# Performance work log

Measured on AMD Instinct MI355X. Metric: run time of the kernel, lower is better.

The kernel has to match this reference:

```python
import jax, jax.numpy as jnp
import numpy as np

B, OBS, H, M, L1, T, A = 16384, 376, 512, 8, 3, 50, 17  # L1 = num_layers - 1
LOG_SQRT_2PI = 0.5 * np.log(2.0 * np.pi).astype(np.float32)


def setup_inputs() -> dict:
    key = jax.random.key(0)
    ks = jax.random.split(key, 16)
    s = lambda fan: 1.0 / np.sqrt(fan).astype(np.float32)
    return {
        "x": jax.random.normal(ks[0], (B, OBS), jnp.float32),
        "task_idx": jax.random.randint(ks[1], (B,), 0, T, jnp.int64),
        "enc_W1": jax.random.normal(ks[2], (OBS, H), jnp.float32) * s(OBS),
        "enc_b1": jnp.zeros((H,), jnp.float32),
        "enc_W2": jax.random.normal(ks[3], (H, H), jnp.float32) * s(H),
        "enc_b2": jnp.zeros((H,), jnp.float32),
        "task_emb": jax.random.normal(ks[4], (T, H), jnp.float32),
        "a_rW": jax.random.normal(ks[5], (L1, H, M * M), jnp.float32) * s(H),
        "a_rb": jnp.zeros((L1, M * M), jnp.float32),
        "c_rW": jax.random.normal(ks[6], (L1, H, M * M), jnp.float32) * s(H),
        "c_rb": jnp.zeros((L1, M * M), jnp.float32),
        "a_W": jax.random.normal(ks[7], (L1, M, H, H), jnp.float32) * s(H),
        "a_b": jnp.zeros((L1, M, H), jnp.float32),
        "a_Wf": jax.random.normal(ks[8], (M, H, A), jnp.float32) * 0.01,
        "a_bf": jnp.zeros((M, A), jnp.float32),
        "c_W": jax.random.normal(ks[9], (L1, M, H, H), jnp.float32) * s(H),
        "c_b": jnp.zeros((L1, M, H), jnp.float32),
        "c_Wf": jax.random.normal(ks[10], (M, H, 1), jnp.float32) * s(H),
        "c_bf": jnp.zeros((M, 1), jnp.float32),
        "actor_logstd": jnp.zeros((1, A), jnp.float32),
    }


def _routing(context, rW, rb):
    # context: [B,H]; rW: [L1,H,M*M] -> list of [B,M,M] softmax routing probs
    rel = jax.nn.relu(context)
    probs = []
    for l in range(L1):
        logits = (rel @ rW[l] + rb[l]).reshape(-1, M, M)
        probs.append(jax.nn.softmax(logits, axis=2))
    return probs


def _base(f_s, probs, W, b, Wf, bf):
    # f_s: [B,H]; W: [L1,M,H,H]; Wf: [M,H,out]
    g = jnp.broadcast_to(f_s[:, None, :], (f_s.shape[0], M, H))  # [B,M,H]
    for l in range(L1):
        outs = jax.nn.relu(jnp.einsum("bmh,mhk->bmk", g, W[l]) + b[l])  # [B,M,H]
        g = jnp.einsum("bij,bjh->bih", probs[l], outs)  # soft combine
    final = jnp.einsum("bmh,mhk->bmk", g, Wf) + bf  # [B,M,out]
    return final.sum(axis=1)


def reference(x, task_idx, enc_W1, enc_b1, enc_W2, enc_b2, task_emb,
              a_rW, a_rb, c_rW, c_rb, a_W, a_b, a_Wf, a_bf,
              c_W, c_b, c_Wf, c_bf, actor_logstd):
    f_s = jnp.tanh(jnp.tanh(x @ enc_W1 + enc_b1) @ enc_W2 + enc_b2)  # [B,H]
    h_z = task_emb[task_idx]  # [B,H]
    context = f_s * h_z

    value = _base(f_s, _routing(context, c_rW, c_rb), c_W, c_b, c_Wf, c_bf)  # [B,1]
    mean = _base(f_s, _routing(context, a_rW, a_rb), a_W, a_b, a_Wf, a_bf)   # [B,A]

    # deterministic action (sample=False): action = mean
    logstd = jnp.broadcast_to(actor_logstd, mean.shape)
    log_prob = (-logstd - LOG_SQRT_2PI).sum(axis=1)          # N.log_prob(mean).sum(1)
    entropy = (0.5 + LOG_SQRT_2PI + logstd).sum(axis=1)
    # concat (action, log_prob, entropy, value) -> [B, A+3]
    return jnp.concatenate([mean, log_prob[:, None], entropy[:, None], value], axis=1)
```

## Files before the change

### kernel.cpp

```cpp
#include <hip/hip_runtime.h>
#include <hip/hip_bf16.h>

typedef float f32x4 __attribute__((ext_vector_type(4)));
typedef float f32x2 __attribute__((ext_vector_type(2)));
typedef int   i32x4 __attribute__((ext_vector_type(4)));
typedef int   i32x8 __attribute__((ext_vector_type(8)));

#define LOG_SQRT_2PI 0.91893853320467274f

static constexpr int BSZ  = 16384;
static constexpr int OBSN = 376;
static constexpr int HD   = 512;
static constexpr int NACT = 17;

__device__ __forceinline__ unsigned char f2fp8(float v) {
  return (unsigned char)(__builtin_amdgcn_cvt_pk_fp8_f32(v, v, 0, false) & 0xFF);
}

__device__ __forceinline__ void xcd_map(int id, int gx, int gy, int& bx, int& by, int& bz) {
  int p = id & 7, l = id >> 3;
  bx = l % gx;
  int g = (l / gx) * 8 + p;
  by = g % gy;
  bz = g / gy;
}


__global__ void k_cvt_pad8(const float* __restrict__ src, unsigned char* __restrict__ dst) {
  long i = (long)blockIdx.x * 256 + threadIdx.x;
  if (i >= (long)BSZ * HD) return;
  long r = i >> 9;
  int  c = (int)(i & 511);
  dst[i] = f2fp8(c < OBSN ? src[r * OBSN + c] : 0.f);
}

__global__ void k_packT8(const float* __restrict__ src, unsigned char* __restrict__ dst,
                         int K, int N, int Kpad, long sstride, long dstride, float scale) {
  __shared__ float t[32][33];
  src += (long)blockIdx.z * sstride;
  dst += (long)blockIdx.z * dstride;
  int k0 = blockIdx.y * 32, n0 = blockIdx.x * 32;
#pragma unroll
  for (int ii = 0; ii < 4; ++ii) {
    int i = ii * 8 + threadIdx.y;
    int k = k0 + i, n = n0 + threadIdx.x;
    t[i][threadIdx.x] = (k < K && n < N) ? src[(long)k * N + n] : 0.f;
  }
  __syncthreads();
#pragma unroll
  for (int ii = 0; ii < 4; ++ii) {
    int i = ii * 8 + threadIdx.y;
    int n = n0 + i, k = k0 + threadIdx.x;
    if (n < N && k < Kpad) dst[(long)n * Kpad + k] = f2fp8(scale * t[threadIdx.x][i]);
  }
}

__global__ void k_packw8(const float* __restrict__ aW, const float* __restrict__ cW,
                         unsigned char* __restrict__ dst) {
  __shared__ float t[32][33];
  const int z = blockIdx.z;
  const float* src = (z < 24) ? aW + (long)z * 262144 : cW + (long)(z - 24) * 262144;
  unsigned char* d = dst + (long)z * 262144;
  int k0 = blockIdx.y * 32, n0 = blockIdx.x * 32;
#pragma unroll
  for (int ii = 0; ii < 4; ++ii) {
    int i = ii * 8 + threadIdx.y;
    t[i][threadIdx.x] = src[(long)(k0 + i) * 512 + n0 + threadIdx.x];
  }
  __syncthreads();
#pragma unroll
  for (int ii = 0; ii < 4; ++ii) {
    int i = ii * 8 + threadIdx.y;
    d[(long)(n0 + i) * 512 + k0 + threadIdx.x] = f2fp8(16.f * t[threadIdx.x][i]);
  }
}

__global__ void k_packwf8(const float* __restrict__ aWf, const float* __restrict__ cWf,
                          unsigned char* __restrict__ dsta, unsigned char* __restrict__ dstc) {
  int i = blockIdx.x * 256 + threadIdx.x;
  int n = i >> 12, k = i & 4095;
  dsta[i] = (n < NACT) ? f2fp8(64.f * aWf[(long)k * NACT + n]) : (unsigned char)0;
  dstc[i] = (n < 1)    ? f2fp8(64.f * cWf[k])                  : (unsigned char)0;
}

__global__ void k_pack_rb(const float* __restrict__ a_rb, const float* __restrict__ c_rb,
                          float* __restrict__ rb) {
  int i = threadIdx.x;
  rb[i] = (i < 192) ? a_rb[i] : c_rb[i - 192];
}

__global__ void k_sum_bf(const float* __restrict__ a_bf, const float* __restrict__ c_bf,
                         float* __restrict__ sa, float* __restrict__ sc) {
  int a = threadIdx.x;
  if (a < NACT) { float s = 0.f; for (int m = 0; m < 8; ++m) s += a_bf[m * NACT + a]; sa[a] = s; }
  if (a == 0)   { float s = 0.f; for (int m = 0; m < 8; ++m) s += c_bf[m];            sc[0] = s; }
}

template <int OP>
__global__ __launch_bounds__(256)
void k_gemm8(const unsigned char* __restrict__ A, const unsigned char* __restrict__ Bt,
             void* __restrict__ Cv, const float* __restrict__ bias,
             int N, int K, int lda, int ldc, int gx, int gy,
             int a_zoff, int b_zoff, int c_zoff, int bias_zoff,
             const int* __restrict__ tidx, const float* __restrict__ temb,
             unsigned char* __restrict__ out2) {
  __shared__ alignas(16) unsigned char sA[128 * 128];
  __shared__ alignas(16) unsigned char sB[128 * 128];
  int bx, by, z;
  xcd_map(blockIdx.x, gx, gy, bx, by, z);
  A  += (long)z * a_zoff;
  Bt += (long)z * b_zoff;
  const int tid  = threadIdx.x;
  const int wave = tid >> 6, lane = tid & 63;
  const int wr = (wave >> 1) * 64, wc = (wave & 1) * 64;
  const int row0 = by * 128, col0 = bx * 128;
  const int lcol = lane & 15, quad = lane >> 4;
  const int sw7 = lcol & 7;
  const int c0 = ((2 * quad)     ^ sw7) * 16;
  const int c1 = ((2 * quad + 1) ^ sw7) * 16;

  f32x4 acc[4][4] = {};

  for (int kt = 0; kt < K; kt += 128) {
#pragma unroll
    for (int i = 0; i < 4; ++i) {
      int u = i * 256 + tid;
      int r = u >> 3, gc = (u & 7) ^ (r & 7);
      const unsigned char* ga = A + (long)(row0 + r) * lda + kt + gc * 16;
      __builtin_amdgcn_global_load_lds((const __attribute__((address_space(1))) void*)ga,
                                       (__attribute__((address_space(3))) void*)&sA[u * 16], 16, 0, 0);
    }
#pragma unroll
    for (int i = 0; i < 4; ++i) {
      int u = i * 256 + tid;
      int r = u >> 3, gc = (u & 7) ^ (r & 7);
      const unsigned char* gb = Bt + (long)(col0 + r) * K + kt + gc * 16;
      __builtin_amdgcn_global_load_lds((const __attribute__((address_space(1))) void*)gb,
                                       (__attribute__((address_space(3))) void*)&sB[u * 16], 16, 0, 0);
    }
    __syncthreads();
    i32x8 af[4], bv[4];
#pragma unroll
    for (int t = 0; t < 4; ++t) {
      int ra = (wr + t * 16 + lcol) * 128;
      int rb = (wc + t * 16 + lcol) * 128;
      i32x4 alo = *(const i32x4*)&sA[ra + c0];
      i32x4 ahi = *(const i32x4*)&sA[ra + c1];
      i32x4 blo = *(const i32x4*)&sB[rb + c0];
      i32x4 bhi = *(const i32x4*)&sB[rb + c1];
      af[t] = (i32x8){alo[0], alo[1], alo[2], alo[3], ahi[0], ahi[1], ahi[2], ahi[3]};
      bv[t] = (i32x8){blo[0], blo[1], blo[2], blo[3], bhi[0], bhi[1], bhi[2], bhi[3]};
    }
#pragma unroll
    for (int mi = 0; mi < 4; ++mi)
#pragma unroll
      for (int ni = 0; ni < 4; ++ni)
        acc[mi][ni] = __builtin_amdgcn_mfma_scale_f32_16x16x128_f8f6f4(
            bv[ni], af[mi], acc[mi][ni], 0, 0, 0, 0x7F, 0, 0x7F);
    __syncthreads();
  }

#pragma unroll
  for (int ni = 0; ni < 4; ++ni) {
    int colb = col0 + wc + ni * 16 + quad * 4;
    if (colb >= N) continue;
    float4 bw = *(const float4*)&bias[(long)z * bias_zoff + colb];
#pragma unroll
    for (int mi = 0; mi < 4; ++mi) {
      int rowg = row0 + wr + mi * 16 + lcol;
      float v0 = acc[mi][ni][0] * 0.0625f + bw.x;
      float v1 = acc[mi][ni][1] * 0.0625f + bw.y;
      float v2 = acc[mi][ni][2] * 0.0625f + bw.z;
      float v3 = acc[mi][ni][3] * 0.0625f + bw.w;
      long idx = (long)rowg * ldc + (long)z * c_zoff + colb;
      if (OP == 1) {
        float t0 = tanhf(v0), t1 = tanhf(v1), t2 = tanhf(v2), t3 = tanhf(v3);
        unsigned d = __builtin_amdgcn_cvt_pk_fp8_f32(t0, t1, 0, false);
        d = __builtin_amdgcn_cvt_pk_fp8_f32(t2, t3, d, true);
        *(unsigned*)&((unsigned char*)Cv)[idx] = d;
      } else if (OP == 5) {
        float t0 = tanhf(v0), t1 = tanhf(v1), t2 = tanhf(v2), t3 = tanhf(v3);
        unsigned d = __builtin_amdgcn_cvt_pk_fp8_f32(t0, t1, 0, false);
        d = __builtin_amdgcn_cvt_pk_fp8_f32(t2, t3, d, true);
        *(unsigned*)&((unsigned char*)Cv)[idx] = d;
        int tk = tidx[rowg];
        float4 te = *(const float4*)&temb[(long)tk * HD + colb];
        unsigned e = __builtin_amdgcn_cvt_pk_fp8_f32(fmaxf(t0 * te.x, 0.f), fmaxf(t1 * te.y, 0.f), 0, false);
        e = __builtin_amdgcn_cvt_pk_fp8_f32(fmaxf(t2 * te.z, 0.f), fmaxf(t3 * te.w, 0.f), e, true);
        *(unsigned*)&out2[idx] = e;
      } else if (OP == 4) {
        float mx = fmaxf(fmaxf(v0, v1), fmaxf(v2, v3));
        mx = fmaxf(mx, __shfl_xor(mx, 16));
        float e0 = __expf(v0 - mx), e1 = __expf(v1 - mx), e2 = __expf(v2 - mx), e3 = __expf(v3 - mx);
        float s = e0 + e1 + e2 + e3;
        s += __shfl_xor(s, 16);
        float inv = 1.f / s;
        *(float4*)&((float*)Cv)[idx] = make_float4(e0 * inv, e1 * inv, e2 * inv, e3 * inv);
      }
    }
  }
}

__global__ __launch_bounds__(512, 2)
void k_gemm256(const unsigned char* __restrict__ A, const unsigned char* __restrict__ Bt,
               unsigned char* __restrict__ C, const float* __restrict__ bias,
               int K, int lda, int ldc, int gx, int gy,
               int a_zoff, int b_zoff, int c_zoff, int bias_zoff) {
  __shared__ alignas(16) unsigned char sA[2][256 * 128];
  __shared__ alignas(16) unsigned char sB[2][256 * 128];
  int bx, by, z;
  xcd_map(blockIdx.x, gx, gy, bx, by, z);
  A  += (long)z * a_zoff;
  Bt += (long)z * b_zoff;
  const int tid  = threadIdx.x;
  const int wave = tid >> 6, lane = tid & 63;
  const int wr = (wave >> 2) * 128;
  const int wc = (wave & 3) * 64;
  const int row0 = by * 256, col0 = bx * 256;
  const int lcol = lane & 15, quad = lane >> 4;
  const int sw7 = lcol & 7;
  const int c0 = ((2 * quad)     ^ sw7) * 16;
  const int c1 = ((2 * quad + 1) ^ sw7) * 16;

  f32x4 acc[8][4] = {};

  auto stage = [&](int kt, int p) {
#pragma unroll
    for (int i = 0; i < 4; ++i) {
      int u = i * 512 + tid;
      int r = u >> 3, gc = (u & 7) ^ (r & 7);
      const unsigned char* ga = A + (long)(row0 + r) * lda + kt + gc * 16;
      __builtin_amdgcn_global_load_lds((const __attribute__((address_space(1))) void*)ga,
                                       (__attribute__((address_space(3))) void*)&sA[p][u * 16], 16, 0, 0);
    }
#pragma unroll
    for (int i = 0; i < 4; ++i) {
      int u = i * 512 + tid;
      int r = u >> 3, gc = (u & 7) ^ (r & 7);
      const unsigned char* gb = Bt + (long)(col0 + r) * K + kt + gc * 16;
      __builtin_amdgcn_global_load_lds((const __attribute__((address_space(1))) void*)gb,
                                       (__attribute__((address_space(3))) void*)&sB[p][u * 16], 16, 0, 0);
    }
  };

  stage(0, 0);
  __syncthreads();
  int p = 0;
  for (int kt = 0; kt < K; kt += 128) {
    if (kt + 128 < K) stage(kt + 128, p ^ 1);
    i32x8 bv[4];
#pragma unroll
    for (int ni = 0; ni < 4; ++ni) {
      int rb = (wc + ni * 16 + lcol) * 128;
      i32x4 blo = *(const i32x4*)&sB[p][rb + c0];
      i32x4 bhi = *(const i32x4*)&sB[p][rb + c1];
      bv[ni] = (i32x8){blo[0], blo[1], blo[2], blo[3], bhi[0], bhi[1], bhi[2], bhi[3]};
    }
#pragma unroll
    for (int mi = 0; mi < 8; ++mi) {
      int ra = (wr + mi * 16 + lcol) * 128;
      i32x4 alo = *(const i32x4*)&sA[p][ra + c0];
      i32x4 ahi = *(const i32x4*)&sA[p][ra + c1];
      i32x8 af = (i32x8){alo[0], alo[1], alo[2], alo[3], ahi[0], ahi[1], ahi[2], ahi[3]};
      __builtin_amdgcn_s_setprio(1);
#pragma unroll
      for (int ni = 0; ni < 4; ++ni)
        acc[mi][ni] = __builtin_amdgcn_mfma_scale_f32_16x16x128_f8f6f4(
            bv[ni], af, acc[mi][ni], 0, 0, 0, 0x7F, 0, 0x7F);
      __builtin_amdgcn_s_setprio(0);
    }
    __syncthreads();
    p ^= 1;
  }

#pragma unroll
  for (int ni = 0; ni < 4; ++ni) {
    int colb = col0 + wc + ni * 16 + quad * 4;
    float4 bw = *(const float4*)&bias[(long)z * bias_zoff + colb];
#pragma unroll
    for (int mi = 0; mi < 8; ++mi) {
      int rowg = row0 + wr + mi * 16 + lcol;
      float v0 = fmaxf(acc[mi][ni][0] * 0.0625f + bw.x, 0.f);
      float v1 = fmaxf(acc[mi][ni][1] * 0.0625f + bw.y, 0.f);
      float v2 = fmaxf(acc[mi][ni][2] * 0.0625f + bw.z, 0.f);
      float v3 = fmaxf(acc[mi][ni][3] * 0.0625f + bw.w, 0.f);
      unsigned d = __builtin_amdgcn_cvt_pk_fp8_f32(v0, v1, 0, false);
      d = __builtin_amdgcn_cvt_pk_fp8_f32(v2, v3, d, true);
      *(unsigned*)&C[(long)rowg * ldc + (long)z * c_zoff + colb] = d;
    }
  }
}

__global__ __launch_bounds__(256)
void k_combine8(const unsigned char* __restrict__ outs, const float* __restrict__ probs,
                unsigned char* __restrict__ g, int poff) {
  __shared__ float P[4][64];
  const int w = threadIdx.x >> 6, l = threadIdx.x & 63;
  const long b = (long)blockIdx.x * 4 + w;
  P[w][l] = probs[b * 384 + poff + l];
  __syncthreads();
  const unsigned char* ob = outs + b * 4096 + l * 8;
  float o[8][8];
#pragma unroll
  for (int j = 0; j < 8; ++j) {
    uint2 v = *(const uint2*)(ob + j * 512);
    f32x2 p01 = __builtin_amdgcn_cvt_pk_f32_fp8(v.x, false);
    f32x2 p23 = __builtin_amdgcn_cvt_pk_f32_fp8(v.x, true);
    f32x2 p45 = __builtin_amdgcn_cvt_pk_f32_fp8(v.y, false);
    f32x2 p67 = __builtin_amdgcn_cvt_pk_f32_fp8(v.y, true);
    o[j][0] = p01.x; o[j][1] = p01.y; o[j][2] = p23.x; o[j][3] = p23.y;
    o[j][4] = p45.x; o[j][5] = p45.y; o[j][6] = p67.x; o[j][7] = p67.y;
  }
  unsigned char* gb = g + b * 4096 + l * 8;
#pragma unroll
  for (int i = 0; i < 8; ++i) {
    float a[8] = {};
#pragma unroll
    for (int j = 0; j < 8; ++j) {
      float pw = P[w][i * 8 + j];
#pragma unroll
      for (int c = 0; c < 8; ++c) a[c] += pw * o[j][c];
    }
    unsigned int lo = __builtin_amdgcn_cvt_pk_fp8_f32(a[0], a[1], 0, false);
    lo = __builtin_amdgcn_cvt_pk_fp8_f32(a[2], a[3], lo, true);
    unsigned int hi = __builtin_amdgcn_cvt_pk_fp8_f32(a[4], a[5], 0, false);
    hi = __builtin_amdgcn_cvt_pk_fp8_f32(a[6], a[7], hi, true);
    *(uint2*)(gb + i * 512) = make_uint2(lo, hi);
  }
}

template <int NOUT>
__global__ __launch_bounds__(256)
void k_head8(const unsigned char* __restrict__ A, const unsigned char* __restrict__ Bt,
             const float* __restrict__ bsum, float* __restrict__ out, int ooff) {
  __shared__ alignas(16) unsigned char sA[64 * 64];
  __shared__ alignas(16) unsigned char sB[32 * 64];
  const int tid = threadIdx.x;
  const int wave = tid >> 6, lane = tid & 63;
  const int row0 = blockIdx.x * 64;
  const int lcol = lane & 15, quad = lane >> 4;
  const int sw = (lcol >> 1) & 3;
  const int co0 = (((quad >> 1)    ) ^ sw) * 16 + (quad & 1) * 8;
  const int co1 = (((quad >> 1) + 2) ^ sw) * 16 + (quad & 1) * 8;
  f32x4 acc[2] = {};

  for (int kt = 0; kt < 4096; kt += 64) {
    {
      int r = tid >> 2, gc = (tid & 3) ^ ((tid >> 3) & 3);
      const unsigned char* ga = A + (long)(row0 + r) * 4096 + kt + gc * 16;
      __builtin_amdgcn_global_load_lds((const __attribute__((address_space(1))) void*)ga,
                                       (__attribute__((address_space(3))) void*)&sA[tid * 16], 16, 0, 0);
    }
    if (tid < 128) {
      int r = tid >> 2, gc = (tid & 3) ^ ((tid >> 3) & 3);
      const unsigned char* gb = Bt + (long)r * 4096 + kt + gc * 16;
      __builtin_amdgcn_global_load_lds((const __attribute__((address_space(1))) void*)gb,
                                       (__attribute__((address_space(3))) void*)&sB[tid * 16], 16, 0, 0);
    }
    __syncthreads();
    long af[2], bv[2][2];
    int ra = (wave * 16 + lcol) * 64;
    af[0] = *(const long*)&sA[ra + co0];
    af[1] = *(const long*)&sA[ra + co1];
#pragma unroll
    for (int ni = 0; ni < 2; ++ni) {
      int rb = (ni * 16 + lcol) * 64;
      bv[0][ni] = *(const long*)&sB[rb + co0];
      bv[1][ni] = *(const long*)&sB[rb + co1];
    }
#pragma unroll
    for (int kk = 0; kk < 2; ++kk)
#pragma unroll
      for (int ni = 0; ni < 2; ++ni)
        acc[ni] = __builtin_amdgcn_mfma_f32_16x16x32_fp8_fp8(af[kk], bv[kk][ni], acc[ni], 0, 0, 0);
    __syncthreads();
  }

#pragma unroll
  for (int ni = 0; ni < 2; ++ni) {
    int col = ni * 16 + lcol;
    if (col >= NOUT) continue;
#pragma unroll
    for (int r = 0; r < 4; ++r) {
      int row = row0 + wave * 16 + quad * 4 + r;
      out[(long)row * 20 + ooff + col] = acc[ni][r] * 0.015625f + bsum[col];
    }
  }
}

__global__ void k_logstd(const float* __restrict__ ls, float* __restrict__ out) {
  float lp = 0.f, ent = 0.f;
#pragma unroll
  for (int a = 0; a < NACT; ++a) {
    float v = ls[a];
    lp  += -v - LOG_SQRT_2PI;
    ent += 0.5f + LOG_SQRT_2PI + v;
  }
  long b = (long)blockIdx.x * 256 + threadIdx.x;
  if (b < BSZ) { out[b * 20 + 17] = lp; out[b * 20 + 18] = ent; }
}


extern "C" void kernel_launch(void* const* d_in, const int* in_sizes, int n_in,
                              void* d_out, int out_size, void* d_ws, size_t ws_size,
                              hipStream_t stream) {
  const float* x        = (const float*)d_in[0];
  const int*   task_idx = (const int*)d_in[1];
  const float* enc_W1   = (const float*)d_in[2];
  const float* enc_b1   = (const float*)d_in[3];
  const float* enc_W2   = (const float*)d_in[4];
  const float* enc_b2   = (const float*)d_in[5];
  const float* task_emb = (const float*)d_in[6];
  const float* a_rW     = (const float*)d_in[7];
  const float* a_rb     = (const float*)d_in[8];
  const float* c_rW     = (const float*)d_in[9];
  const float* c_rb     = (const float*)d_in[10];
  const float* a_W      = (const float*)d_in[11];
  const float* a_b      = (const float*)d_in[12];
  const float* a_Wf     = (const float*)d_in[13];
  const float* a_bf     = (const float*)d_in[14];
  const float* c_W      = (const float*)d_in[15];
  const float* c_b      = (const float*)d_in[16];
  const float* c_Wf     = (const float*)d_in[17];
  const float* c_bf     = (const float*)d_in[18];
  const float* logstd   = (const float*)d_in[19];
  float* out = (float*)d_out;

  char* ws = (char*)d_ws;
  size_t off = 0;
  auto carve = [&](size_t bytes) {
    char* p = ws + off;
    off += (bytes + 255) & ~(size_t)255;
    return p;
  };
  unsigned char* W8 = (unsigned char*)carve((size_t)48 * 262144);
  unsigned char* W1T8 = (unsigned char*)carve((size_t)512 * 512);
  unsigned char* W2T8 = (unsigned char*)carve((size_t)512 * 512);
  unsigned char* rWT8 = (unsigned char*)carve((size_t)384 * 512);
  float* rball = (float*)carve(384 * 4);
  unsigned char* WfaT8 = (unsigned char*)carve((size_t)32 * 4096);
  unsigned char* WfcT8 = (unsigned char*)carve((size_t)32 * 4096);
  float* bfa   = (float*)carve(128 * 4);
  float* bfc   = (float*)carve(128 * 4);
  unsigned char* fs8 = (unsigned char*)carve((size_t)BSZ * HD);
  float* lgt   = (float*)carve((size_t)BSZ * 384 * 4);

  size_t remain = (ws_size > off) ? (ws_size - off) : 0;
  int Bc = 4096;
  for (int cand = BSZ; cand > 4096; cand >>= 1)
    if ((size_t)2 * cand * 4096 <= remain) { Bc = cand; break; }
  size_t half = (size_t)Bc * 4096;
  unsigned char* bufA8 = (unsigned char*)carve(half);
  unsigned char* bufB8 = (unsigned char*)carve(half);
  unsigned char* x8   = bufA8;
  unsigned char* h18  = bufB8;
  unsigned char* rel8 = bufA8;

  dim3 tb(32, 8);

  k_cvt_pad8<<<(int)(((long)BSZ * HD + 255) / 256), 256, 0, stream>>>(x, x8);
  k_packT8<<<dim3(16, 16, 1), tb, 0, stream>>>(enc_W1, W1T8, OBSN, 512, 512, 0, 0, 16.f);
  k_packT8<<<dim3(16, 16, 1), tb, 0, stream>>>(enc_W2, W2T8, 512, 512, 512, 0, 0, 16.f);
  k_packT8<<<dim3(2, 16, 3),  tb, 0, stream>>>(a_rW, rWT8,             512, 64, 512, 512 * 64, 64 * 512, 16.f);
  k_packT8<<<dim3(2, 16, 3),  tb, 0, stream>>>(c_rW, rWT8 + 192 * 512, 512, 64, 512, 512 * 64, 64 * 512, 16.f);
  k_packw8<<<dim3(16, 16, 48), tb, 0, stream>>>(a_W, c_W, W8);
  k_packwf8<<<512, 256, 0, stream>>>(a_Wf, c_Wf, WfaT8, WfcT8);
  k_pack_rb<<<1, 384, 0, stream>>>(a_rb, c_rb, rball);
  k_sum_bf<<<1, 32, 0, stream>>>(a_bf, c_bf, bfa, bfc);

  const int GY = BSZ / 128;
  k_gemm8<1><<<4 * GY, 256, 0, stream>>>(x8, W1T8, h18, enc_b1, 512, 512, 512, 512,
                                         4, GY, 0, 0, 0, 0, nullptr, nullptr, nullptr);
  k_gemm8<5><<<4 * GY, 256, 0, stream>>>(h18, W2T8, fs8, enc_b2, 512, 512, 512, 512,
                                         4, GY, 0, 0, 0, 0, task_idx, task_emb, rel8);
  k_gemm8<4><<<3 * GY, 256, 0, stream>>>(rel8, rWT8, lgt, rball, 384, 512, 512, 384,
                                         3, GY, 0, 0, 0, 0, nullptr, nullptr, nullptr);

  const size_t wz8 = (size_t)8 * 262144;
  const unsigned char* W8a = W8;
  const unsigned char* W8c = W8 + (size_t)24 * 262144;
  for (int c0 = 0; c0 < BSZ; c0 += Bc) {
    const unsigned char* fs_c = fs8 + (long)c0 * 512;
    const float* pr_c  = lgt + (long)c0 * 384;
    float*       out_c = out + (long)c0 * 20;
    const int gy = Bc / 256;

    k_gemm256<<<16 * gy, 512, 0, stream>>>(fs_c, W8c, bufA8, c_b, 512, 512, 4096,
                                           16, gy, 0, 0, 0, 0);
    k_combine8<<<Bc / 4, 256, 0, stream>>>(bufA8, pr_c, bufB8, 192 + 0);
    k_gemm256<<<2 * gy * 8, 512, 0, stream>>>(bufB8, W8c + 1 * wz8, bufA8, c_b + 4096,
                                              512, 4096, 4096, 2, gy, 512, 262144, 512, 512);
    k_combine8<<<Bc / 4, 256, 0, stream>>>(bufA8, pr_c, bufB8, 192 + 64);
    k_gemm256<<<2 * gy * 8, 512, 0, stream>>>(bufB8, W8c + 2 * wz8, bufA8, c_b + 8192,
                                              512, 4096, 4096, 2, gy, 512, 262144, 512, 512);
    k_combine8<<<Bc / 4, 256, 0, stream>>>(bufA8, pr_c, bufB8, 192 + 128);
    k_head8<1><<<Bc / 64, 256, 0, stream>>>(bufB8, WfcT8, bfc, out_c, 19);

    k_gemm256<<<16 * gy, 512, 0, stream>>>(fs_c, W8a, bufA8, a_b, 512, 512, 4096,
                                           16, gy, 0, 0, 0, 0);
    k_combine8<<<Bc / 4, 256, 0, stream>>>(bufA8, pr_c, bufB8, 0);
    k_gemm256<<<2 * gy * 8, 512, 0, stream>>>(bufB8, W8a + 1 * wz8, bufA8, a_b + 4096,
                                              512, 4096, 4096, 2, gy, 512, 262144, 512, 512);
    k_combine8<<<Bc / 4, 256, 0, stream>>>(bufA8, pr_c, bufB8, 64);
    k_gemm256<<<2 * gy * 8, 512, 0, stream>>>(bufB8, W8a + 2 * wz8, bufA8, a_b + 8192,
                                              512, 4096, 4096, 2, gy, 512, 262144, 512, 512);
    k_combine8<<<Bc / 4, 256, 0, stream>>>(bufA8, pr_c, bufB8, 128);
    k_head8<NACT><<<Bc / 64, 256, 0, stream>>>(bufB8, WfaT8, bfa, out_c, 0);
  }

  k_logstd<<<BSZ / 256, 256, 0, stream>>>(logstd, out);
}
```

Before: 842.4 us.

## Restructure fp8 GEMM main loop into fine-grained interleaved load/MFMA phases

Splits each K-tile iteration of the 256x256 fp8 GEMM into four phases. Each phase interleaves a pair of global-to-LDS prefetch issues for the next tile, the LDS fragment reads and a block of eight MFMAs. Explicit vmcnt/lgkmcnt waits and raw s_barriers replace the single __syncthreads per tile, so memory traffic is spread across the compute and stalls are smaller. The cost is many more barriers per tile and hand-tuned wait counts that must stay correct for the pipelining to remain safe.

```diff
diff --git a/kernel.cpp b/kernel.cpp
--- a/kernel.cpp
+++ b/kernel.cpp
@@ -12,6 +12,9 @@
 static constexpr int OBSN = 376;
 static constexpr int HD   = 512;
 static constexpr int NACT = 17;
+
+#define S_VMCNT(n) asm volatile("s_waitcnt vmcnt(" #n ")" ::: "memory")
+#define S_LGKM0()  asm volatile("s_waitcnt lgkmcnt(0)" ::: "memory")
 
 __device__ __forceinline__ unsigned char f2fp8(float v) {
   return (unsigned char)(__builtin_amdgcn_cvt_pk_fp8_f32(v, v, 0, false) & 0xFF);
@@ -206,8 +209,8 @@
                unsigned char* __restrict__ C, const float* __restrict__ bias,
                int K, int lda, int ldc, int gx, int gy,
                int a_zoff, int b_zoff, int c_zoff, int bias_zoff) {
-  __shared__ alignas(16) unsigned char sA[2][256 * 128];
-  __shared__ alignas(16) unsigned char sB[2][256 * 128];
+  __shared__ alignas(16) unsigned char sA[2 * 32768];
+  __shared__ alignas(16) unsigned char sB[2 * 32768];
   int bx, by, z;
   xcd_map(blockIdx.x, gx, gy, bx, by, z);
   A  += (long)z * a_zoff;
@@ -223,55 +226,85 @@
   const int c1 = ((2 * quad + 1) ^ sw7) * 16;
 
   f32x4 acc[8][4] = {};
-
-  auto stage = [&](int kt, int p) {
-#pragma unroll
-    for (int i = 0; i < 4; ++i) {
-      int u = i * 512 + tid;
-      int r = u >> 3, gc = (u & 7) ^ (r & 7);
+  i32x8 af[4], bv[4];
+
+  auto issue = [&](int c, int kt, int pq) {
+    int u = ((c & 3) << 9) + tid;
+    int r = u >> 3, gc = (u & 7) ^ (r & 7);
+    if (c < 4) {
       const unsigned char* ga = A + (long)(row0 + r) * lda + kt + gc * 16;
       __builtin_amdgcn_global_load_lds((const __attribute__((address_space(1))) void*)ga,
-                                       (__attribute__((address_space(3))) void*)&sA[p][u * 16], 16, 0, 0);
-    }
-#pragma unroll
-    for (int i = 0; i < 4; ++i) {
-      int u = i * 512 + tid;
-      int r = u >> 3, gc = (u & 7) ^ (r & 7);
+          (__attribute__((address_space(3))) void*)&sA[(pq << 15) + u * 16], 16, 0, 0);
+    } else {
       const unsigned char* gb = Bt + (long)(col0 + r) * K + kt + gc * 16;
       __builtin_amdgcn_global_load_lds((const __attribute__((address_space(1))) void*)gb,
-                                       (__attribute__((address_space(3))) void*)&sB[p][u * 16], 16, 0, 0);
+          (__attribute__((address_space(3))) void*)&sB[(pq << 15) + u * 16], 16, 0, 0);
     }
   };
-
-  stage(0, 0);
-  __syncthreads();
+  auto rd_a = [&](int idx, int pb, int rowoff) {
+    int ra = pb + (wr + rowoff + lcol) * 128;
+    i32x4 lo = *(const i32x4*)&sA[ra + c0];
+    i32x4 hi = *(const i32x4*)&sA[ra + c1];
+    af[idx] = (i32x8){lo[0], lo[1], lo[2], lo[3], hi[0], hi[1], hi[2], hi[3]};
+  };
+  auto rd_b = [&](int ni, int pb) {
+    int rb = pb + (wc + ni * 16 + lcol) * 128;
+    i32x4 lo = *(const i32x4*)&sB[rb + c0];
+    i32x4 hi = *(const i32x4*)&sB[rb + c1];
+    bv[ni] = (i32x8){lo[0], lo[1], lo[2], lo[3], hi[0], hi[1], hi[2], hi[3]};
+  };
+
+#define MFMA8(MIB, NIB)                                                                    \
+  __builtin_amdgcn_s_setprio(1);                                                           \
+  _Pragma("unroll")                                                                        \
+  for (int q2 = 0; q2 < 4; ++q2) {                                                         \
+    acc[(MIB) + q2][(NIB)]     = __builtin_amdgcn_mfma_scale_f32_16x16x128_f8f6f4(         \
+        bv[(NIB)], af[q2], acc[(MIB) + q2][(NIB)], 0, 0, 0, 0x7F, 0, 0x7F);                \
+    acc[(MIB) + q2][(NIB) + 1] = __builtin_amdgcn_mfma_scale_f32_16x16x128_f8f6f4(         \
+        bv[(NIB) + 1], af[q2], acc[(MIB) + q2][(NIB) + 1], 0, 0, 0, 0x7F, 0, 0x7F);        \
+  }                                                                                        \
+  __builtin_amdgcn_s_setprio(0);
+
+  const int NT = K >> 7;
+  issue(4, 0, 0); issue(5, 0, 0); issue(6, 0, 0); issue(7, 0, 0);
+  issue(0, 0, 0); issue(2, 0, 0); issue(1, 0, 0); issue(3, 0, 0);
+  S_VMCNT(2);
+  __builtin_amdgcn_s_barrier();
+
   int p = 0;
-  for (int kt = 0; kt < K; kt += 128) {
-    if (kt + 128 < K) stage(kt + 128, p ^ 1);
-    i32x8 bv[4];
-#pragma unroll
-    for (int ni = 0; ni < 4; ++ni) {
-      int rb = (wc + ni * 16 + lcol) * 128;
-      i32x4 blo = *(const i32x4*)&sB[p][rb + c0];
-      i32x4 bhi = *(const i32x4*)&sB[p][rb + c1];
-      bv[ni] = (i32x8){blo[0], blo[1], blo[2], blo[3], bhi[0], bhi[1], bhi[2], bhi[3]};
-    }
-#pragma unroll
-    for (int mi = 0; mi < 8; ++mi) {
-      int ra = (wr + mi * 16 + lcol) * 128;
-      i32x4 alo = *(const i32x4*)&sA[p][ra + c0];
-      i32x4 ahi = *(const i32x4*)&sA[p][ra + c1];
-      i32x8 af = (i32x8){alo[0], alo[1], alo[2], alo[3], ahi[0], ahi[1], ahi[2], ahi[3]};
-      __builtin_amdgcn_s_setprio(1);
-#pragma unroll
-      for (int ni = 0; ni < 4; ++ni)
-        acc[mi][ni] = __builtin_amdgcn_mfma_scale_f32_16x16x128_f8f6f4(
-            bv[ni], af, acc[mi][ni], 0, 0, 0, 0x7F, 0, 0x7F);
-      __builtin_amdgcn_s_setprio(0);
-    }
-    __syncthreads();
-    p ^= 1;
-  }
+#pragma unroll 1
+  for (int t = 0; t < NT; ++t, p ^= 1) {
+    const int pb = p << 15, q = p ^ 1;
+    const int ktn = (t + 1) << 7;
+    const bool pf = (t + 1 < NT);
+    if (pf) { issue(4, ktn, q); issue(5, ktn, q); }
+    rd_a(0, pb, 0); rd_a(1, pb, 16); rd_a(2, pb, 32); rd_a(3, pb, 48);
+    rd_b(0, pb); rd_b(1, pb);
+    __builtin_amdgcn_s_barrier();
+    S_LGKM0(); __builtin_amdgcn_sched_barrier(0);
+    MFMA8(0, 0);
+    __builtin_amdgcn_s_barrier();
+    if (pf) { issue(6, ktn, q); issue(7, ktn, q); }
+    rd_b(2, pb); rd_b(3, pb);
+    if (pf) S_VMCNT(4); else S_VMCNT(0);
+    __builtin_amdgcn_s_barrier();
+    S_LGKM0(); __builtin_amdgcn_sched_barrier(0);
+    MFMA8(0, 2);
+    __builtin_amdgcn_s_barrier();
+    if (pf) { issue(0, ktn, q); issue(2, ktn, q); }
+    rd_a(0, pb, 64); rd_a(1, pb, 80); rd_a(2, pb, 96); rd_a(3, pb, 112);
+    __builtin_amdgcn_s_barrier();
+    S_LGKM0(); __builtin_amdgcn_sched_barrier(0);
+    MFMA8(4, 0);
+    __builtin_amdgcn_s_barrier();
+    if (pf) { issue(1, ktn, q); issue(3, ktn, q); }
+    if (pf) S_VMCNT(2); else S_VMCNT(0);
+    __builtin_amdgcn_s_barrier();
+    __builtin_amdgcn_sched_barrier(0);
+    MFMA8(4, 2);
+    __builtin_amdgcn_s_barrier();
+  }
+#undef MFMA8
 
 #pragma unroll
   for (int ni = 0; ni < 4; ++ni) {
```

Result: slower. 921.5 us (+9.4%).
